# Kernel optimization log

Measured on AMD Instinct MI355X. Metric: run time of the kernel, lower is better.

Reference implementation:

```python
import jax, jax.numpy as jnp
import numpy as np

B, S, C, H = 256, 512, 64, 128  # batch, seq_len, input channels, LSTM hidden


def setup_inputs() -> dict:
    key = jax.random.key(0)
    ks = jax.random.split(key, 9)
    s = 1.0 / np.sqrt(H)  # torch nn.LSTM init: U(-1/sqrt(H), 1/sqrt(H))
    u = lambda k, shape: jax.random.uniform(k, shape, jnp.float32, -s, s)
    return {
        "x": jax.random.normal(ks[0], (B, S, C), jnp.float32),
        # layer 0 (input size C)
        "Wih0": u(ks[1], (4 * H, C)),
        "Whh0": u(ks[2], (4 * H, H)),
        "bih0": u(ks[3], (4 * H,)),
        "bhh0": u(ks[4], (4 * H,)),
        # layer 1 (input size H)
        "Wih1": u(ks[5], (4 * H, H)),
        "Whh1": u(ks[6], (4 * H, H)),
        "bih1": u(ks[7], (4 * H,)),
        "bhh1": u(ks[8], (4 * H,)),
    }


def _lstm_layer(x, Wih, Whh, bih, bhh):
    """x: (S, B, in) -> outputs h_t for all t: (S, B, H). Torch gate order i,f,g,o."""
    Hh = Whh.shape[1]
    # Input-to-hidden GEMM hoisted out of the recurrence (batched over S).
    xg = jnp.einsum('sbc,gc->sbg', x, Wih) + bih + bhh  # (S, B, 4H)

    def step(carry, xt):
        h, c = carry
        g = xt + h @ Whh.T  # (B, 4H)
        i, f, gg, o = jnp.split(g, 4, axis=-1)
        i = jax.nn.sigmoid(i)
        f = jax.nn.sigmoid(f)
        gg = jnp.tanh(gg)
        o = jax.nn.sigmoid(o)
        c = f * c + i * gg
        h = o * jnp.tanh(c)
        return (h, c), h

    h0 = jnp.zeros((x.shape[1], Hh), x.dtype)
    _, ys = jax.lax.scan(step, (h0, h0), xg)
    return ys


def reference(x, Wih0, Whh0, bih0, bhh0, Wih1, Whh1, bih1, bhh1):
    xs = jnp.transpose(x, (1, 0, 2))  # (B,S,C) -> (S,B,C), matching x.permute(1,0,2)
    y1 = _lstm_layer(xs, Wih0, Whh0, bih0, bhh0)
    y2 = _lstm_layer(y1, Wih1, Whh1, bih1, bhh1)
    return y2[-1]  # x[-1, :, :]: last timestep of top layer, (B, H)
```

## Files before the change

### kernel.cpp

```cpp
#include <hip/hip_runtime.h>
#include <cstdint>
#include <cstddef>


#define S_LEN 512
#define B_SZ  256
#define C_IN  64
#define HDIM  128
#define CH    16
#define NPAIR 64

using short8  = __attribute__((ext_vector_type(8))) short;
using float4v = __attribute__((ext_vector_type(4))) float;

__device__ __forceinline__ unsigned short f2b(float f) {
    union { float f; unsigned int u; } v; v.f = f;
    unsigned int u = v.u;
    return (unsigned short)((u + 0x7FFFu + ((u >> 16) & 1u)) >> 16);
}
__device__ __forceinline__ float sig_(float x) {
    return __builtin_amdgcn_rcpf(1.0f + __builtin_amdgcn_exp2f(x * -1.442695041f));
}
__device__ __forceinline__ float tanh_(float x) {
    return 1.0f - 2.0f * __builtin_amdgcn_rcpf(1.0f + __builtin_amdgcn_exp2f(x * 2.885390082f));
}

__global__ void prep_kernel(const float* __restrict__ x,
                            const float* __restrict__ wih0, const float* __restrict__ whh0,
                            const float* __restrict__ bih0, const float* __restrict__ bhh0,
                            const float* __restrict__ wih1, const float* __restrict__ whh1,
                            const float* __restrict__ bih1, const float* __restrict__ bhh1,
                            unsigned short* __restrict__ whh0_b, unsigned short* __restrict__ wih0_b,
                            unsigned short* __restrict__ whh1_b, unsigned short* __restrict__ wih1_b,
                            float* __restrict__ bias0, float* __restrict__ bias1,
                            unsigned short* __restrict__ xb) {
    int i = blockIdx.x * blockDim.x + threadIdx.x;
    if (i < B_SZ * S_LEN * C_IN) xb[i] = f2b(x[i]);
    if (i < 4 * HDIM * HDIM) {
        whh0_b[i] = f2b(whh0[i]);
        whh1_b[i] = f2b(whh1[i]);
        wih1_b[i] = f2b(wih1[i]);
    }
    if (i < 4 * HDIM * C_IN) wih0_b[i] = f2b(wih0[i]);
    if (i < 4 * HDIM) {
        bias0[i] = bih0[i] + bhh0[i];
        bias1[i] = bih1[i] + bhh1[i];
    }
}

template<int KIN, bool IS_L0>
__device__ __forceinline__ void lstm_layer(
    unsigned short* hbuf,
    float* xgf,
    const unsigned short* __restrict__ in_seq,
    const unsigned short* __restrict__ wih_b,
    const unsigned short* __restrict__ whh_b,
    const float* __restrict__ bias,
    unsigned short* __restrict__ y1,
    float* __restrict__ final_out,
    int* __restrict__ flags, int blk) {
    constexpr int KK = KIN / 32;
    const int tid = threadIdx.x;
    const int w = tid >> 6, L = tid & 63, q = L >> 4, r = L & 15;
    const int boff = blk * 4, j0 = w * 16, j = j0 + r;

    short8 whh[4][4], wih[4][KK];
    float bias_s[4];
#pragma unroll
    for (int g = 0; g < 4; ++g) {
        const int nrow = g * HDIM + j;
#pragma unroll
        for (int kk = 0; kk < 4; ++kk)
            whh[g][kk] = *(const short8*)(whh_b + (size_t)nrow * HDIM + kk * 32 + q * 8);
#pragma unroll
        for (int kk = 0; kk < KK; ++kk)
            wih[g][kk] = *(const short8*)(wih_b + (size_t)nrow * KIN + kk * 32 + q * 8);
        bias_s[g] = bias[g * HDIM + j];
    }

    for (int idx = tid; idx < 4096; idx += 512) hbuf[idx] = 0;
    float cf = 0.f;

    short8 af[KK];
    auto loadA = [&](int ch, int sub) {
        const int t = ch * CH + sub * 4 + (r >> 2);
        const int b = boff + (r & 3);
        const unsigned short* base;
        if constexpr (IS_L0) base = in_seq + ((size_t)b * S_LEN + t) * C_IN;
        else                 base = in_seq + ((size_t)t * B_SZ + b) * HDIM;
#pragma unroll
        for (int kk = 0; kk < KK; ++kk)
            af[kk] = *(const short8*)(base + kk * 32 + q * 8);
    };

    if constexpr (IS_L0) loadA(0, 0);

    for (int ch = 0; ch < 32; ++ch) {
        if constexpr (!IS_L0) {
            if (tid == 0)
                while (__hip_atomic_load(flags + blk * 32 + ch, __ATOMIC_ACQUIRE,
                                         __HIP_MEMORY_SCOPE_AGENT) != ch + 1)
                    __builtin_amdgcn_s_sleep(2);
            __syncthreads();
            loadA(ch, 0);
        }
#pragma unroll 1
        for (int sub = 0; sub < 4; ++sub) {
#pragma unroll
            for (int g = 0; g < 4; ++g) {
                float4v a = {0.f, 0.f, 0.f, 0.f};
#pragma unroll
                for (int kk = 0; kk < KK; ++kk)
                    a = __builtin_amdgcn_mfma_f32_16x16x32_bf16(af[kk], wih[g][kk], a, 0, 0, 0);
#pragma unroll
                for (int rr = 0; rr < 4; ++rr)
                    xgf[((q * 8 + w) * 64 + rr * 16 + r) * 4 + g] = a[rr] + bias_s[g];
            }
            if (sub < 3) loadA(ch, sub + 1);
            else if (IS_L0 && ch < 31) loadA(ch + 1, 0);
            __syncthreads();

#pragma unroll
            for (int sl = 0; sl < 4; ++sl) {
                const int s = sub * 4 + sl;
                const int t = ch * CH + s;
                unsigned short* cur = hbuf + (s & 1) * 2048;
                unsigned short* nxt = hbuf + ((s & 1) ^ 1) * 2048;
                short8 hfrag[4];
#pragma unroll
                for (int kk = 0; kk < 4; ++kk)
                    hfrag[kk] = *(const short8*)(cur + ((kk * 4 + q) * 16 + r) * 8);
                const float4v xv = ((const float4v*)xgf)[(sl * 8 + w) * 64 + L];
                float4v a0 = {xv[0], 0.f, 0.f, 0.f};
                float4v a1 = {xv[1], 0.f, 0.f, 0.f};
                float4v a2 = {xv[2], 0.f, 0.f, 0.f};
                float4v a3 = {xv[3], 0.f, 0.f, 0.f};
#pragma unroll
                for (int kk = 0; kk < 4; ++kk) {
                    a0 = __builtin_amdgcn_mfma_f32_16x16x32_bf16(hfrag[kk], whh[0][kk], a0, 0, 0, 0);
                    a1 = __builtin_amdgcn_mfma_f32_16x16x32_bf16(hfrag[kk], whh[1][kk], a1, 0, 0, 0);
                    a2 = __builtin_amdgcn_mfma_f32_16x16x32_bf16(hfrag[kk], whh[2][kk], a2, 0, 0, 0);
                    a3 = __builtin_amdgcn_mfma_f32_16x16x32_bf16(hfrag[kk], whh[3][kk], a3, 0, 0, 0);
                }
                const float iv = sig_(a0[0]);
                const float fv = sig_(a1[0]);
                const float gv = tanh_(a2[0]);
                const float ov = sig_(a3[0]);
                cf = fv * cf + iv * gv;
                const float hv = ov * tanh_(cf);
                nxt[(j >> 3) * 128 + 32 * q + (j & 7)] = f2b(hv);
                if constexpr (!IS_L0) {
                    if (t == S_LEN - 1)
                        final_out[(size_t)(boff + q) * HDIM + j] = hv;
                }
                __syncthreads();
                if constexpr (IS_L0) {
                    if (tid < 64)
                        *(short8*)(y1 + ((size_t)t * B_SZ + boff + (L >> 4)) * HDIM + (L & 15) * 8)
                            = *(const short8*)(nxt + (L & 15) * 128 + (L >> 4) * 32);
                }
            }
        }
        if constexpr (IS_L0) {
            __threadfence();
            __syncthreads();
            if (tid == 0)
                __hip_atomic_store(flags + blk * 32 + ch, ch + 1, __ATOMIC_RELEASE,
                                   __HIP_MEMORY_SCOPE_AGENT);
        }
    }
}

__global__ __launch_bounds__(512, 2)
void lstm_pipe(const unsigned short* __restrict__ xb,
               const unsigned short* __restrict__ wih0_b, const unsigned short* __restrict__ whh0_b,
               const float* __restrict__ bias0,
               const unsigned short* __restrict__ wih1_b, const unsigned short* __restrict__ whh1_b,
               const float* __restrict__ bias1,
               unsigned short* __restrict__ y1, float* __restrict__ out,
               int* __restrict__ flags) {
    __shared__ __align__(16) unsigned short hbuf[2 * 2048];
    __shared__ __align__(16) float xgf[4 * 8 * 64 * 4];
    if (blockIdx.x < NPAIR)
        lstm_layer<C_IN, true>(hbuf, xgf, xb, wih0_b, whh0_b, bias0, y1, nullptr,
                               flags, blockIdx.x);
    else
        lstm_layer<HDIM, false>(hbuf, xgf, y1, wih1_b, whh1_b, bias1, nullptr, out,
                                flags, blockIdx.x - NPAIR);
}


extern "C" void kernel_launch(void* const* d_in, const int* in_sizes, int n_in,
                              void* d_out, int out_size, void* d_ws, size_t ws_size,
                              hipStream_t stream) {
    const float* x    = (const float*)d_in[0];
    const float* wih0 = (const float*)d_in[1];
    const float* whh0 = (const float*)d_in[2];
    const float* bih0 = (const float*)d_in[3];
    const float* bhh0 = (const float*)d_in[4];
    const float* wih1 = (const float*)d_in[5];
    const float* whh1 = (const float*)d_in[6];
    const float* bih1 = (const float*)d_in[7];
    const float* bhh1 = (const float*)d_in[8];

    char* ws = (char*)d_ws;
    unsigned short* whh0_b = (unsigned short*)(ws + 0);
    unsigned short* wih0_b = (unsigned short*)(ws + 131072);
    unsigned short* whh1_b = (unsigned short*)(ws + 196608);
    unsigned short* wih1_b = (unsigned short*)(ws + 327680);
    float*          bias0  = (float*)(ws + 458752);
    float*          bias1  = (float*)(ws + 460800);
    int*            flags  = (int*)(ws + 462848);
    unsigned short* xb     = (unsigned short*)(ws + 524288);
    unsigned short* y1     = (unsigned short*)(ws + 17301504);

    hipMemsetAsync(flags, 0, 8192, stream);

    prep_kernel<<<(B_SZ * S_LEN * C_IN + 255) / 256, 256, 0, stream>>>(
        x, wih0, whh0, bih0, bhh0, wih1, whh1, bih1, bhh1,
        whh0_b, wih0_b, whh1_b, wih1_b, bias0, bias1, xb);

    lstm_pipe<<<dim3(2 * NPAIR), dim3(512), 0, stream>>>(
        xb, wih0_b, whh0_b, bias0, wih1_b, whh1_b, bias1, y1, (float*)d_out, flags);
}
```

Baseline: 784.4 us.

## Use 4-slot LDS h ring and batch y1 stores per four-step quad

Replaces the double-buffered hidden-state buffer with a four-slot ring in shared memory. Layer-0 blocks now write four timesteps of h to global y1 at once (256 threads) at the start of the next quad, instead of 64 threads writing after every step's barrier. The A-operand input loads are double-buffered across quads (afA/afB) so the next quad's input is prefetched earlier. The per-step final_out branch is replaced by a single store after the loop. This trims work off the serial recurrence critical path, at the cost of more LDS and a more intricate flag/slot ordering.

```diff
diff --git a/kernel.cpp b/kernel.cpp
--- a/kernel.cpp
+++ b/kernel.cpp
@@ -7,7 +7,6 @@
 #define B_SZ  256
 #define C_IN  64
 #define HDIM  128
-#define CH    16
 #define NPAIR 64
 
 using short8  = __attribute__((ext_vector_type(8))) short;
@@ -50,7 +49,7 @@
 
 template<int KIN, bool IS_L0>
 __device__ __forceinline__ void lstm_layer(
-    unsigned short* hbuf,
+    unsigned short* ring,
     float* xgf,
     const unsigned short* __restrict__ in_seq,
     const unsigned short* __restrict__ wih_b,
@@ -62,7 +61,7 @@
     constexpr int KK = KIN / 32;
     const int tid = threadIdx.x;
     const int w = tid >> 6, L = tid & 63, q = L >> 4, r = L & 15;
-    const int boff = blk * 4, j0 = w * 16, j = j0 + r;
+    const int boff = blk * 4, j = w * 16 + r;
 
     short8 whh[4][4], wih[4][KK];
     float bias_s[4];
@@ -78,12 +77,14 @@
         bias_s[g] = bias[g * HDIM + j];
     }
 
-    for (int idx = tid; idx < 4096; idx += 512) hbuf[idx] = 0;
-    float cf = 0.f;
-
-    short8 af[KK];
-    auto loadA = [&](int ch, int sub) {
-        const int t = ch * CH + sub * 4 + (r >> 2);
+    for (int idx = tid; idx < 4 * 2048; idx += 512) ring[idx] = 0;
+    float cf = 0.f, hv_last = 0.f;
+
+    const int su = tid >> 6, ii = (tid >> 4) & 3, cc = tid & 15;
+    const unsigned short* ysrc = ring + ((su + 1) & 3) * 2048 + cc * 128 + ii * 32;
+
+    auto loadA = [&](int t0, short8* af) {
+        const int t = t0 + (r >> 2);
         const int b = boff + (r & 3);
         const unsigned short* base;
         if constexpr (IS_L0) base = in_seq + ((size_t)b * S_LEN + t) * C_IN;
@@ -93,81 +94,101 @@
             af[kk] = *(const short8*)(base + kk * 32 + q * 8);
     };
 
-    if constexpr (IS_L0) loadA(0, 0);
-
-    for (int ch = 0; ch < 32; ++ch) {
-        if constexpr (!IS_L0) {
-            if (tid == 0)
-                while (__hip_atomic_load(flags + blk * 32 + ch, __ATOMIC_ACQUIRE,
-                                         __HIP_MEMORY_SCOPE_AGENT) != ch + 1)
-                    __builtin_amdgcn_s_sleep(2);
+    if constexpr (!IS_L0) {
+        if (tid == 0)
+            while (__hip_atomic_load(flags + blk * 32, __ATOMIC_ACQUIRE,
+                                     __HIP_MEMORY_SCOPE_AGENT) != 1)
+                __builtin_amdgcn_s_sleep(2);
+    }
+    __syncthreads();
+
+    short8 afA[KK], afB[KK];
+    loadA(0, afA);
+
+    auto quad = [&](int pt, short8* afu, short8* afl) {
+        if constexpr (IS_L0) {
+            if (pt > 0 && tid < 256) {
+                short8 v = *(const short8*)ysrc;
+                *(short8*)(y1 + ((size_t)(pt - 4 + su) * B_SZ + boff + ii) * HDIM + cc * 8) = v;
+            }
+            if (pt > 0 && (pt & 15) == 0) {
+                __threadfence();
+                __syncthreads();
+                if (tid == 0)
+                    __hip_atomic_store(flags + blk * 32 + (pt >> 4) - 1, (pt >> 4),
+                                       __ATOMIC_RELEASE, __HIP_MEMORY_SCOPE_AGENT);
+            }
+        } else {
+            if (pt + 4 < S_LEN && ((pt + 4) & 15) == 0) {
+                const int ch = (pt + 4) >> 4;
+                if (tid == 0)
+                    while (__hip_atomic_load(flags + blk * 32 + ch, __ATOMIC_ACQUIRE,
+                                             __HIP_MEMORY_SCOPE_AGENT) != ch + 1)
+                        __builtin_amdgcn_s_sleep(2);
+                __syncthreads();
+            }
+        }
+        if (pt + 4 < S_LEN) loadA(pt + 4, afl);
+#pragma unroll
+        for (int g = 0; g < 4; ++g) {
+            float4v a = {0.f, 0.f, 0.f, 0.f};
+#pragma unroll
+            for (int kk = 0; kk < KK; ++kk)
+                a = __builtin_amdgcn_mfma_f32_16x16x32_bf16(afu[kk], wih[g][kk], a, 0, 0, 0);
+#pragma unroll
+            for (int rr = 0; rr < 4; ++rr)
+                xgf[((q * 8 + w) * 64 + rr * 16 + r) * 4 + g] = a[rr] + bias_s[g];
+        }
+        __syncthreads();
+
+#pragma unroll
+        for (int sl = 0; sl < 4; ++sl) {
+            short8 hfrag[4];
+#pragma unroll
+            for (int kk = 0; kk < 4; ++kk)
+                hfrag[kk] = *(const short8*)(ring + sl * 2048 + ((kk * 4 + q) * 16 + r) * 8);
+            const float4v xv = *(const float4v*)(xgf + ((sl * 8 + w) * 64 + L) * 4);
+            float4v a0 = {xv[0], 0.f, 0.f, 0.f};
+            float4v a1 = {xv[1], 0.f, 0.f, 0.f};
+            float4v a2 = {xv[2], 0.f, 0.f, 0.f};
+            float4v a3 = {xv[3], 0.f, 0.f, 0.f};
+#pragma unroll
+            for (int kk = 0; kk < 4; ++kk) {
+                a0 = __builtin_amdgcn_mfma_f32_16x16x32_bf16(hfrag[kk], whh[0][kk], a0, 0, 0, 0);
+                a1 = __builtin_amdgcn_mfma_f32_16x16x32_bf16(hfrag[kk], whh[1][kk], a1, 0, 0, 0);
+                a2 = __builtin_amdgcn_mfma_f32_16x16x32_bf16(hfrag[kk], whh[2][kk], a2, 0, 0, 0);
+                a3 = __builtin_amdgcn_mfma_f32_16x16x32_bf16(hfrag[kk], whh[3][kk], a3, 0, 0, 0);
+            }
+            const float iv = sig_(a0[0]);
+            const float fv = sig_(a1[0]);
+            const float gv = tanh_(a2[0]);
+            const float ov = sig_(a3[0]);
+            cf = fv * cf + iv * gv;
+            const float hv = ov * tanh_(cf);
+            hv_last = hv;
+            ring[((sl + 1) & 3) * 2048 + (j >> 3) * 128 + 32 * q + (j & 7)] = f2b(hv);
             __syncthreads();
-            loadA(ch, 0);
-        }
+        }
+    };
+
 #pragma unroll 1
-        for (int sub = 0; sub < 4; ++sub) {
-#pragma unroll
-            for (int g = 0; g < 4; ++g) {
-                float4v a = {0.f, 0.f, 0.f, 0.f};
-#pragma unroll
-                for (int kk = 0; kk < KK; ++kk)
-                    a = __builtin_amdgcn_mfma_f32_16x16x32_bf16(af[kk], wih[g][kk], a, 0, 0, 0);
-#pragma unroll
-                for (int rr = 0; rr < 4; ++rr)
-                    xgf[((q * 8 + w) * 64 + rr * 16 + r) * 4 + g] = a[rr] + bias_s[g];
-            }
-            if (sub < 3) loadA(ch, sub + 1);
-            else if (IS_L0 && ch < 31) loadA(ch + 1, 0);
-            __syncthreads();
-
-#pragma unroll
-            for (int sl = 0; sl < 4; ++sl) {
-                const int s = sub * 4 + sl;
-                const int t = ch * CH + s;
-                unsigned short* cur = hbuf + (s & 1) * 2048;
-                unsigned short* nxt = hbuf + ((s & 1) ^ 1) * 2048;
-                short8 hfrag[4];
-#pragma unroll
-                for (int kk = 0; kk < 4; ++kk)
-                    hfrag[kk] = *(const short8*)(cur + ((kk * 4 + q) * 16 + r) * 8);
-                const float4v xv = ((const float4v*)xgf)[(sl * 8 + w) * 64 + L];
-                float4v a0 = {xv[0], 0.f, 0.f, 0.f};
-                float4v a1 = {xv[1], 0.f, 0.f, 0.f};
-                float4v a2 = {xv[2], 0.f, 0.f, 0.f};
-                float4v a3 = {xv[3], 0.f, 0.f, 0.f};
-#pragma unroll
-                for (int kk = 0; kk < 4; ++kk) {
-                    a0 = __builtin_amdgcn_mfma_f32_16x16x32_bf16(hfrag[kk], whh[0][kk], a0, 0, 0, 0);
-                    a1 = __builtin_amdgcn_mfma_f32_16x16x32_bf16(hfrag[kk], whh[1][kk], a1, 0, 0, 0);
-                    a2 = __builtin_amdgcn_mfma_f32_16x16x32_bf16(hfrag[kk], whh[2][kk], a2, 0, 0, 0);
-                    a3 = __builtin_amdgcn_mfma_f32_16x16x32_bf16(hfrag[kk], whh[3][kk], a3, 0, 0, 0);
-                }
-                const float iv = sig_(a0[0]);
-                const float fv = sig_(a1[0]);
-                const float gv = tanh_(a2[0]);
-                const float ov = sig_(a3[0]);
-                cf = fv * cf + iv * gv;
-                const float hv = ov * tanh_(cf);
-                nxt[(j >> 3) * 128 + 32 * q + (j & 7)] = f2b(hv);
-                if constexpr (!IS_L0) {
-                    if (t == S_LEN - 1)
-                        final_out[(size_t)(boff + q) * HDIM + j] = hv;
-                }
-                __syncthreads();
-                if constexpr (IS_L0) {
-                    if (tid < 64)
-                        *(short8*)(y1 + ((size_t)t * B_SZ + boff + (L >> 4)) * HDIM + (L & 15) * 8)
-                            = *(const short8*)(nxt + (L & 15) * 128 + (L >> 4) * 32);
-                }
-            }
-        }
-        if constexpr (IS_L0) {
-            __threadfence();
-            __syncthreads();
-            if (tid == 0)
-                __hip_atomic_store(flags + blk * 32 + ch, ch + 1, __ATOMIC_RELEASE,
-                                   __HIP_MEMORY_SCOPE_AGENT);
-        }
+    for (int tt = 0; tt < S_LEN; tt += 8) {
+        quad(tt, afA, afB);
+        quad(tt + 4, afB, afA);
+    }
+
+    if constexpr (IS_L0) {
+        if (tid < 256) {
+            short8 v = *(const short8*)ysrc;
+            *(short8*)(y1 + ((size_t)(S_LEN - 4 + su) * B_SZ + boff + ii) * HDIM + cc * 8) = v;
+        }
+        __threadfence();
+        __syncthreads();
+        if (tid == 0)
+            __hip_atomic_store(flags + blk * 32 + 31, 32,
+                               __ATOMIC_RELEASE, __HIP_MEMORY_SCOPE_AGENT);
+    } else {
+        final_out[(size_t)(boff + q) * HDIM + j] = hv_last;
     }
 }
 
@@ -179,13 +200,13 @@
                const float* __restrict__ bias1,
                unsigned short* __restrict__ y1, float* __restrict__ out,
                int* __restrict__ flags) {
-    __shared__ __align__(16) unsigned short hbuf[2 * 2048];
+    __shared__ __align__(16) unsigned short ring[4 * 2048];
     __shared__ __align__(16) float xgf[4 * 8 * 64 * 4];
     if (blockIdx.x < NPAIR)
-        lstm_layer<C_IN, true>(hbuf, xgf, xb, wih0_b, whh0_b, bias0, y1, nullptr,
+        lstm_layer<C_IN, true>(ring, xgf, xb, wih0_b, whh0_b, bias0, y1, nullptr,
                                flags, blockIdx.x);
     else
-        lstm_layer<HDIM, false>(hbuf, xgf, y1, wih1_b, whh1_b, bias1, nullptr, out,
+        lstm_layer<HDIM, false>(ring, xgf, y1, wih1_b, whh1_b, bias1, nullptr, out,
                                 flags, blockIdx.x - NPAIR);
 }
 
```

Result: no change. 789.7 us (+0.7%).

## Replace per-step block barriers with per-wave LDS flag handshakes and 4-slot h ring

Applied to the files above, without the earlier changes.

Removes the __syncthreads after every timestep. Each wave now publishes its slice of h into a 4-deep LDS ring buffer and signals a workgroup-scope flag, and consumer waves spin only on the flags for the K-slices they need. The input projection is folded into the per-step MFMA chain and the next timestep's input is prefetched from registers, so the LDS xg staging buffer is gone. Layer-1 gating now counts per-wave atomic increments. This cuts barrier cost on the serial recurrence at the price of more MFMAs per step and spin-wait traffic on LDS flags.

```diff
diff --git a/kernel.cpp b/kernel.cpp
--- a/kernel.cpp
+++ b/kernel.cpp
@@ -7,7 +7,6 @@
 #define B_SZ  256
 #define C_IN  64
 #define HDIM  128
-#define CH    16
 #define NPAIR 64
 
 using short8  = __attribute__((ext_vector_type(8))) short;
@@ -49,20 +48,20 @@
 }
 
 template<int KIN, bool IS_L0>
-__device__ __forceinline__ void lstm_layer(
-    unsigned short* hbuf,
-    float* xgf,
+__device__ __forceinline__ void lstm_wave(
+    unsigned short* ring,
+    int* flagsL,
     const unsigned short* __restrict__ in_seq,
     const unsigned short* __restrict__ wih_b,
     const unsigned short* __restrict__ whh_b,
     const float* __restrict__ bias,
     unsigned short* __restrict__ y1,
-    float* __restrict__ final_out,
-    int* __restrict__ flags, int blk) {
+    float* __restrict__ out,
+    int* __restrict__ flags_g, int blk) {
     constexpr int KK = KIN / 32;
     const int tid = threadIdx.x;
     const int w = tid >> 6, L = tid & 63, q = L >> 4, r = L & 15;
-    const int boff = blk * 4, j0 = w * 16, j = j0 + r;
+    const int boff = blk * 4, j = w * 16 + r;
 
     short8 whh[4][4], wih[4][KK];
     float bias_s[4];
@@ -78,95 +77,97 @@
         bias_s[g] = bias[g * HDIM + j];
     }
 
-    for (int idx = tid; idx < 4096; idx += 512) hbuf[idx] = 0;
+    for (int idx = tid; idx < 4 * 2048; idx += 512) ring[idx] = 0;
+    if (tid < 8) flagsL[tid] = 0;
+    __syncthreads();
+
     float cf = 0.f;
-
-    short8 af[KK];
-    auto loadA = [&](int ch, int sub) {
-        const int t = ch * CH + sub * 4 + (r >> 2);
-        const int b = boff + (r & 3);
-        const unsigned short* base;
-        if constexpr (IS_L0) base = in_seq + ((size_t)b * S_LEN + t) * C_IN;
-        else                 base = in_seq + ((size_t)t * B_SZ + b) * HDIM;
+    const int bload = boff + (r >> 2);
+    const unsigned short* base;
+    size_t tstr;
+    if constexpr (IS_L0) { base = in_seq + (size_t)bload * S_LEN * C_IN + q * 8; tstr = C_IN; }
+    else                 { base = in_seq + (size_t)bload * HDIM + q * 8; tstr = (size_t)B_SZ * HDIM; }
+
+    auto gate = [&](int ch) {
+        if constexpr (!IS_L0) {
+            while (__hip_atomic_load(flags_g + blk * 32 + ch, __ATOMIC_ACQUIRE,
+                                     __HIP_MEMORY_SCOPE_AGENT) < 8)
+                __builtin_amdgcn_s_sleep(1);
+        }
+    };
+    auto loadin = [&](int t, short8* dst) {
 #pragma unroll
         for (int kk = 0; kk < KK; ++kk)
-            af[kk] = *(const short8*)(base + kk * 32 + q * 8);
+            dst[kk] = *(const short8*)(base + (size_t)t * tstr + kk * 32);
     };
 
-    if constexpr (IS_L0) loadA(0, 0);
-
+    gate(0);
+    short8 xcur[KK], xnxt[KK];
+    loadin(0, xcur);
+
+    const int hwr = (j >> 3) * 128 + 32 * q + (j & 7);
+
+#pragma unroll 1
     for (int ch = 0; ch < 32; ++ch) {
-        if constexpr (!IS_L0) {
-            if (tid == 0)
-                while (__hip_atomic_load(flags + blk * 32 + ch, __ATOMIC_ACQUIRE,
-                                         __HIP_MEMORY_SCOPE_AGENT) != ch + 1)
-                    __builtin_amdgcn_s_sleep(2);
-            __syncthreads();
-            loadA(ch, 0);
-        }
-#pragma unroll 1
-        for (int sub = 0; sub < 4; ++sub) {
-#pragma unroll
-            for (int g = 0; g < 4; ++g) {
-                float4v a = {0.f, 0.f, 0.f, 0.f};
-#pragma unroll
-                for (int kk = 0; kk < KK; ++kk)
-                    a = __builtin_amdgcn_mfma_f32_16x16x32_bf16(af[kk], wih[g][kk], a, 0, 0, 0);
-#pragma unroll
-                for (int rr = 0; rr < 4; ++rr)
-                    xgf[((q * 8 + w) * 64 + rr * 16 + r) * 4 + g] = a[rr] + bias_s[g];
-            }
-            if (sub < 3) loadA(ch, sub + 1);
-            else if (IS_L0 && ch < 31) loadA(ch + 1, 0);
-            __syncthreads();
-
-#pragma unroll
-            for (int sl = 0; sl < 4; ++sl) {
-                const int s = sub * 4 + sl;
-                const int t = ch * CH + s;
-                unsigned short* cur = hbuf + (s & 1) * 2048;
-                unsigned short* nxt = hbuf + ((s & 1) ^ 1) * 2048;
-                short8 hfrag[4];
-#pragma unroll
-                for (int kk = 0; kk < 4; ++kk)
-                    hfrag[kk] = *(const short8*)(cur + ((kk * 4 + q) * 16 + r) * 8);
-                const float4v xv = ((const float4v*)xgf)[(sl * 8 + w) * 64 + L];
-                float4v a0 = {xv[0], 0.f, 0.f, 0.f};
-                float4v a1 = {xv[1], 0.f, 0.f, 0.f};
-                float4v a2 = {xv[2], 0.f, 0.f, 0.f};
-                float4v a3 = {xv[3], 0.f, 0.f, 0.f};
-#pragma unroll
-                for (int kk = 0; kk < 4; ++kk) {
-                    a0 = __builtin_amdgcn_mfma_f32_16x16x32_bf16(hfrag[kk], whh[0][kk], a0, 0, 0, 0);
-                    a1 = __builtin_amdgcn_mfma_f32_16x16x32_bf16(hfrag[kk], whh[1][kk], a1, 0, 0, 0);
-                    a2 = __builtin_amdgcn_mfma_f32_16x16x32_bf16(hfrag[kk], whh[2][kk], a2, 0, 0, 0);
-                    a3 = __builtin_amdgcn_mfma_f32_16x16x32_bf16(hfrag[kk], whh[3][kk], a3, 0, 0, 0);
+#pragma unroll 4
+        for (int s = 0; s < 16; ++s) {
+            const int t = ch * 16 + s;
+            const int slotR = ((t + 3) & 3) * 2048;
+            short8 hf[4];
+#pragma unroll
+            for (int kk = 0; kk < 4; ++kk) {
+                while (__hip_atomic_load(flagsL + 2 * kk, __ATOMIC_ACQUIRE,
+                                         __HIP_MEMORY_SCOPE_WORKGROUP) < t ||
+                       __hip_atomic_load(flagsL + 2 * kk + 1, __ATOMIC_ACQUIRE,
+                                         __HIP_MEMORY_SCOPE_WORKGROUP) < t) {}
+                hf[kk] = *(const short8*)(ring + slotR + ((kk * 4 + q) * 16 + r) * 8);
+            }
+            float4v a0 = {bias_s[0], bias_s[0], bias_s[0], bias_s[0]};
+            float4v a1 = {bias_s[1], bias_s[1], bias_s[1], bias_s[1]};
+            float4v a2 = {bias_s[2], bias_s[2], bias_s[2], bias_s[2]};
+            float4v a3 = {bias_s[3], bias_s[3], bias_s[3], bias_s[3]};
+#pragma unroll
+            for (int kk = 0; kk < 4; ++kk) {
+                a0 = __builtin_amdgcn_mfma_f32_16x16x32_bf16(hf[kk], whh[0][kk], a0, 0, 0, 0);
+                a1 = __builtin_amdgcn_mfma_f32_16x16x32_bf16(hf[kk], whh[1][kk], a1, 0, 0, 0);
+                a2 = __builtin_amdgcn_mfma_f32_16x16x32_bf16(hf[kk], whh[2][kk], a2, 0, 0, 0);
+                a3 = __builtin_amdgcn_mfma_f32_16x16x32_bf16(hf[kk], whh[3][kk], a3, 0, 0, 0);
+            }
+#pragma unroll
+            for (int kk = 0; kk < KK; ++kk) {
+                a0 = __builtin_amdgcn_mfma_f32_16x16x32_bf16(xcur[kk], wih[0][kk], a0, 0, 0, 0);
+                a1 = __builtin_amdgcn_mfma_f32_16x16x32_bf16(xcur[kk], wih[1][kk], a1, 0, 0, 0);
+                a2 = __builtin_amdgcn_mfma_f32_16x16x32_bf16(xcur[kk], wih[2][kk], a2, 0, 0, 0);
+                a3 = __builtin_amdgcn_mfma_f32_16x16x32_bf16(xcur[kk], wih[3][kk], a3, 0, 0, 0);
+            }
+            if (s == 15 && ch < 31) gate(ch + 1);
+            const int tn = (t < S_LEN - 1) ? t + 1 : t;
+            loadin(tn, xnxt);
+            const float iv = sig_(a0[0]);
+            const float fv = sig_(a1[0]);
+            const float gv = tanh_(a2[0]);
+            const float ov = sig_(a3[0]);
+            cf = fv * cf + iv * gv;
+            const float hv = ov * tanh_(cf);
+            const unsigned short hb = f2b(hv);
+            ring[(t & 3) * 2048 + hwr] = hb;
+            if constexpr (IS_L0)
+                y1[((size_t)t * B_SZ + boff + q) * HDIM + j] = hb;
+            else if (t == S_LEN - 1)
+                out[(size_t)(boff + q) * HDIM + j] = hv;
+            if (L == 0)
+                __hip_atomic_store(flagsL + w, t + 1, __ATOMIC_RELEASE,
+                                   __HIP_MEMORY_SCOPE_WORKGROUP);
+            if constexpr (IS_L0) {
+                if (s == 15) {
+                    __threadfence();
+                    if (L == 0)
+                        __hip_atomic_fetch_add(flags_g + blk * 32 + ch, 1,
+                                               __ATOMIC_RELEASE, __HIP_MEMORY_SCOPE_AGENT);
                 }
-                const float iv = sig_(a0[0]);
-                const float fv = sig_(a1[0]);
-                const float gv = tanh_(a2[0]);
-                const float ov = sig_(a3[0]);
-                cf = fv * cf + iv * gv;
-                const float hv = ov * tanh_(cf);
-                nxt[(j >> 3) * 128 + 32 * q + (j & 7)] = f2b(hv);
-                if constexpr (!IS_L0) {
-                    if (t == S_LEN - 1)
-                        final_out[(size_t)(boff + q) * HDIM + j] = hv;
-                }
-                __syncthreads();
-                if constexpr (IS_L0) {
-                    if (tid < 64)
-                        *(short8*)(y1 + ((size_t)t * B_SZ + boff + (L >> 4)) * HDIM + (L & 15) * 8)
-                            = *(const short8*)(nxt + (L & 15) * 128 + (L >> 4) * 32);
-                }
-            }
-        }
-        if constexpr (IS_L0) {
-            __threadfence();
-            __syncthreads();
-            if (tid == 0)
-                __hip_atomic_store(flags + blk * 32 + ch, ch + 1, __ATOMIC_RELEASE,
-                                   __HIP_MEMORY_SCOPE_AGENT);
+            }
+#pragma unroll
+            for (int kk = 0; kk < KK; ++kk) xcur[kk] = xnxt[kk];
         }
     }
 }
@@ -178,15 +179,15 @@
                const unsigned short* __restrict__ wih1_b, const unsigned short* __restrict__ whh1_b,
                const float* __restrict__ bias1,
                unsigned short* __restrict__ y1, float* __restrict__ out,
-               int* __restrict__ flags) {
-    __shared__ __align__(16) unsigned short hbuf[2 * 2048];
-    __shared__ __align__(16) float xgf[4 * 8 * 64 * 4];
+               int* __restrict__ flags_g) {
+    __shared__ __align__(16) unsigned short ring[4 * 2048];
+    __shared__ int flagsL[8];
     if (blockIdx.x < NPAIR)
-        lstm_layer<C_IN, true>(hbuf, xgf, xb, wih0_b, whh0_b, bias0, y1, nullptr,
-                               flags, blockIdx.x);
+        lstm_wave<C_IN, true>(ring, flagsL, xb, wih0_b, whh0_b, bias0, y1, nullptr,
+                              flags_g, blockIdx.x);
     else
-        lstm_layer<HDIM, false>(hbuf, xgf, y1, wih1_b, whh1_b, bias1, nullptr, out,
-                                flags, blockIdx.x - NPAIR);
+        lstm_wave<HDIM, false>(ring, flagsL, y1, wih1_b, whh1_b, bias1, nullptr, out,
+                               flags_g, blockIdx.x - NPAIR);
 }
 
 
```

Result: slower. 1.138 ms (+45.1%).
